# Kernel tuning notes

Hardware: AMD Instinct MI355X
Metric: run time of the kernel (lower is better)

The kernel has to match this reference:

```python
import jax, jax.numpy as jnp
import numpy as np

B, S, E = 2, 2048, 2048
H, HKV, KQV = 16, 4, 2048
D = KQV // H            # 128 head dim
KV_DIM = D * HKV        # 512
WINDOW = 256
NEG = jnp.finfo(jnp.float32).min


def setup_inputs() -> dict:
    key = jax.random.key(0)
    ks = jax.random.split(key, 5)
    sc = 0.02
    return {
        "hidden_states": jax.random.normal(ks[0], (B, S, E), jnp.float32),
        "Wq": jax.random.normal(ks[1], (KQV, E), jnp.float32) * sc,
        "Wk": jax.random.normal(ks[2], (KV_DIM, E), jnp.float32) * sc,
        "Wv": jax.random.normal(ks[3], (KV_DIM, E), jnp.float32) * sc,
        "Wo": jax.random.normal(ks[4], (E, KQV), jnp.float32) * sc,
        "bo": jnp.zeros((E,), jnp.float32),
    }


def reference(hidden_states, Wq, Wk, Wv, Wo, bo):
    x = hidden_states
    # projections (nn.Linear: x @ W.T)
    q = (x @ Wq.T).reshape(B, S, H, D).transpose(0, 2, 1, 3)      # [B,H,S,D]
    k = (x @ Wk.T).reshape(B, S, HKV, D).transpose(0, 2, 1, 3)    # [B,HKV,S,D]
    v = (x @ Wv.T).reshape(B, S, HKV, D).transpose(0, 2, 1, 3)

    # faithful reproduction of the module's index_select head expansion:
    # group_sizes are uniform (H % HKV == 0); both query and kv indices are
    # [0]*g + [1]*g + ... so query head i (i < HKV) is duplicated g times.
    idx = jnp.repeat(jnp.arange(HKV), H // HKV)                   # [H]
    qs = q[:, idx]                                                # [B,H,S,D]
    ks = k[:, idx]
    vs = v[:, idx]

    # GPT-Neo style: no 1/sqrt(D) scaling
    scores = jnp.einsum('bhqd,bhkd->bhqk', qs, ks)                # [B,H,S,S]

    i = jnp.arange(S)[:, None]
    j = jnp.arange(S)[None, :]
    # local causal mask: j <= i and j > i - WINDOW
    mask = (j <= i) & (j > i - WINDOW)                            # [S,S]
    scores = jnp.where(mask[None, None], scores, NEG)
    attn = jax.nn.softmax(scores, axis=-1)

    out = jnp.einsum('bhqk,bhkd->bhqd', attn, vs)                 # [B,H,S,D]
    out = out.transpose(0, 2, 1, 3).reshape(B, S, H * D)          # merge heads
    return out @ Wo.T + bo
```

## Files before the change

### kernel.cpp

```cpp
#include <hip/hip_runtime.h>

typedef _Float16 f16;
typedef _Float16 f16x8 __attribute__((ext_vector_type(8)));
typedef _Float16 f16x4 __attribute__((ext_vector_type(4)));
typedef float    f32x4 __attribute__((ext_vector_type(4)));


__device__ __forceinline__ void load_lds16(const void* g, void* l) {
    __builtin_amdgcn_global_load_lds(
        (__attribute__((address_space(1))) void*)(g),
        (__attribute__((address_space(3))) void*)(l), 16, 0, 0);
}

__global__ __launch_bounds__(256)
void cvt_pack(const float* __restrict__ X, const float* __restrict__ Wq,
              const float* __restrict__ Wk, const float* __restrict__ Wv,
              const float* __restrict__ Wo,
              f16* __restrict__ Xp, f16* __restrict__ Wp, f16* __restrict__ Wrp)
{
    const int blk = blockIdx.x, tid = threadIdx.x;
    if (blk < 4096) {
        int cid = blk * 256 + tid;
        int tile = cid >> 8, wc = cid & 255;
        int row = wc >> 2, kc = wc & 3;
        int m = ((tile >> 6) << 6) + row;
        int t = tile & 63;
        int sk = t * 32 + ((kc ^ ((row >> 1) & 3)) << 3);
        const float* s = X + (size_t)m * 2048 + sk;
        float4 a = *(const float4*)(s);
        float4 b = *(const float4*)(s + 4);
        f16x8 o;
        o[0]=(f16)a.x; o[1]=(f16)a.y; o[2]=(f16)a.z; o[3]=(f16)a.w;
        o[4]=(f16)b.x; o[5]=(f16)b.y; o[6]=(f16)b.z; o[7]=(f16)b.w;
        *(f16x8*)(Xp + (size_t)cid * 8) = o;
    } else if (blk < 5632) {
        int wid = (blk - 4096) * 256 + tid;
        int tile = wid >> 9, wc = wid & 511;
        int row = wc >> 2, kc = wc & 3;
        int n = ((tile >> 6) << 7) + row;
        int t = tile & 63;
        int sk = t * 32 + ((kc ^ ((row >> 1) & 3)) << 3);
        const float* src = (n < 512)  ? (Wq + (size_t)n * 2048 + sk)
                         : (n < 1024) ? (Wk + (size_t)(n - 512) * 2048 + sk)
                                      : (Wv + (size_t)(n - 1024) * 2048 + sk);
        float4 a = *(const float4*)(src);
        float4 b = *(const float4*)(src + 4);
        f16x8 o;
        o[0]=(f16)a.x; o[1]=(f16)a.y; o[2]=(f16)a.z; o[3]=(f16)a.w;
        o[4]=(f16)b.x; o[5]=(f16)b.y; o[6]=(f16)b.z; o[7]=(f16)b.w;
        *(f16x8*)(Wp + (size_t)wid * 8) = o;
    } else {
        int rid = (blk - 5632) * 256 + tid;
        int tile = rid >> 9, wc = rid & 511;
        int row = wc >> 2, kc = wc & 3;
        int e = ((tile >> 4) << 7) + row;
        int t = tile & 15;
        int cc = kc ^ ((row >> 1) & 3);
        int c = t * 32 + (cc << 3);
        int g = c >> 7, d0 = c & 127;
        const float* src = Wo + (size_t)e * 2048 + g * 512 + d0;
        float4 a0 = *(const float4*)(src);
        float4 a1 = *(const float4*)(src + 128);
        float4 a2 = *(const float4*)(src + 256);
        float4 a3 = *(const float4*)(src + 384);
        float4 b0 = *(const float4*)(src + 4);
        float4 b1 = *(const float4*)(src + 132);
        float4 b2 = *(const float4*)(src + 260);
        float4 b3 = *(const float4*)(src + 388);
        f16x8 o;
        o[0] = (f16)(a0.x + a1.x + a2.x + a3.x);
        o[1] = (f16)(a0.y + a1.y + a2.y + a3.y);
        o[2] = (f16)(a0.z + a1.z + a2.z + a3.z);
        o[3] = (f16)(a0.w + a1.w + a2.w + a3.w);
        o[4] = (f16)(b0.x + b1.x + b2.x + b3.x);
        o[5] = (f16)(b0.y + b1.y + b2.y + b3.y);
        o[6] = (f16)(b0.z + b1.z + b2.z + b3.z);
        o[7] = (f16)(b0.w + b1.w + b2.w + b3.w);
        *(f16x8*)(Wrp + (size_t)rid * 8) = o;
    }
}

__global__ __launch_bounds__(256)
void qkv_gemm(const f16* __restrict__ Xp, const f16* __restrict__ Wp,
              f16* __restrict__ Qo, f16* __restrict__ Ko, f16* __restrict__ Vo)
{
    const int NSTEP = 64;
    __shared__ __align__(16) f16 S[4][8192];

    const int tid = threadIdx.x;
    const int wave = tid >> 6, lane = tid & 63;
    const int lrow = lane & 15, lquad = lane >> 4;
    const int wr = wave >> 1, wc = wave & 1;

    int id = (int)blockIdx.x;
    int id2 = (id & 7) * 48 + (id >> 3);
    int bx = id2 % 12, by = id2 / 12;
    const int m0 = by * 128;

    const f16* gA0 = Xp + (size_t)(2 * by)     * 131072 + (size_t)tid * 8;
    const f16* gA1 = Xp + (size_t)(2 * by + 1) * 131072 + (size_t)tid * 8;
    const f16* gB0 = Wp + (size_t)bx * 262144 + (size_t)tid * 8;
    const f16* gB1 = Wp + (size_t)bx * 262144 + (size_t)(256 + tid) * 8;
    const int loA0 = tid * 8;
    const int loA1 = (256 + tid) * 8;
    const int loB0 = (512 + tid) * 8;
    const int loB1 = (768 + tid) * 8;

#define QSTAGE(t, buf)                                             \
    {                                                              \
        load_lds16(gA0 + (size_t)(t) * 2048, &S[buf][loA0]);       \
        load_lds16(gA1 + (size_t)(t) * 2048, &S[buf][loA1]);       \
        load_lds16(gB0 + (size_t)(t) * 4096, &S[buf][loB0]);       \
        load_lds16(gB1 + (size_t)(t) * 4096, &S[buf][loB1]);       \
    }

    int aoff[4], boff[4];
#pragma unroll
    for (int t = 0; t < 4; t++) {
        int ra = wr * 64 + t * 16 + lrow;
        aoff[t] = ra * 32 + ((lquad ^ ((ra >> 1) & 3)) << 3);
        int rb = wc * 64 + t * 16 + lrow;
        boff[t] = 4096 + rb * 32 + ((lquad ^ ((rb >> 1) & 3)) << 3);
    }

    f32x4 acc[4][4];
    const f32x4 z4 = {0.f, 0.f, 0.f, 0.f};
#pragma unroll
    for (int i = 0; i < 4; i++) for (int j = 0; j < 4; j++) acc[i][j] = z4;

    QSTAGE(0, 0); QSTAGE(1, 1); QSTAGE(2, 2);

    int buf = 0;
    for (int t = 0; t < NSTEP; ++t) {
        if (t < NSTEP - 2) {
            asm volatile("s_waitcnt vmcnt(8) lgkmcnt(0)" ::: "memory");
        } else if (t == NSTEP - 2) {
            asm volatile("s_waitcnt vmcnt(4) lgkmcnt(0)" ::: "memory");
        } else {
            asm volatile("s_waitcnt vmcnt(0) lgkmcnt(0)" ::: "memory");
        }
        __builtin_amdgcn_s_barrier();
        if (t < NSTEP - 3) QSTAGE(t + 3, (buf + 3) & 3);
        f16x8 af[4], bf[4];
#pragma unroll
        for (int mt = 0; mt < 4; mt++) af[mt] = *(const f16x8*)(&S[buf][aoff[mt]]);
#pragma unroll
        for (int nt = 0; nt < 4; nt++) bf[nt] = *(const f16x8*)(&S[buf][boff[nt]]);
#pragma unroll
        for (int mt = 0; mt < 4; mt++)
#pragma unroll
            for (int nt = 0; nt < 4; nt++)
                acc[mt][nt] = __builtin_amdgcn_mfma_f32_16x16x32_f16(af[mt], bf[nt], acc[mt][nt], 0, 0, 0);
        buf = (buf + 1) & 3;
    }
#undef QSTAGE

    const int z = bx >> 2;
    const int hh = bx & 3;
    if (z == 0) {
#pragma unroll
        for (int mt = 0; mt < 4; mt++) {
            int mbase = m0 + wr * 64 + mt * 16 + lquad * 4;
#pragma unroll
            for (int r = 0; r < 4; r++) {
                int m = mbase + r;
                int bb = m >> 11, s = m & 2047;
#pragma unroll
                for (int nt = 0; nt < 4; nt++) {
                    int d = wc * 64 + nt * 16 + lrow;
                    Qo[(size_t)(((bb * 4 + hh) << 11) + s) * 128 + d] = (f16)acc[mt][nt][r];
                }
            }
        }
    } else if (z == 1) {
#pragma unroll
        for (int mt = 0; mt < 4; mt++) {
            int mbase = m0 + wr * 64 + mt * 16 + lquad * 4;
#pragma unroll
            for (int r = 0; r < 4; r++) {
                int m = mbase + r;
                int bb = m >> 11, s = m & 2047;
                size_t base = ((size_t)(bb * 4 + hh) * 16 + (s >> 7)) * 16384
                            + (size_t)(s & 127) * 128;
#pragma unroll
                for (int nt = 0; nt < 4; nt++) {
                    int d = wc * 64 + nt * 16 + lrow;
                    Ko[base + (((d >> 3) ^ (s & 15)) << 3) + (d & 7)] = (f16)acc[mt][nt][r];
                }
            }
        }
    } else {
#pragma unroll
        for (int mt = 0; mt < 4; mt++) {
            int mbase = m0 + wr * 64 + mt * 16 + lquad * 4;
            int bb = mbase >> 11, s = mbase & 2047;
            int tt = s >> 7, sl = s & 127;
            int gsx = sl >> 3, j0 = sl & 7;
#pragma unroll
            for (int nt = 0; nt < 4; nt++) {
                int d = wc * 64 + nt * 16 + lrow;
                f16x4 pk;
#pragma unroll
                for (int r = 0; r < 4; r++) pk[r] = (f16)acc[mt][nt][r];
                *(f16x4*)(Vo + ((size_t)(bb * 4 + hh) * 16 + tt) * 16384
                             + (size_t)d * 128 + ((gsx ^ (d & 15)) << 3) + j0) = pk;
            }
        }
    }
}

__global__ __launch_bounds__(256)
void attn_win(const f16* __restrict__ Q, const f16* __restrict__ Kp,
              const f16* __restrict__ Vp, f16* __restrict__ AO)
{
    const int h = blockIdx.x;
    const int bg = h & 7, qt = h >> 3;
    const int b = bg >> 2, g = bg & 3;
    const int qbase = qt * 64;
    const int tid = threadIdx.x;
    const int wave = tid >> 6, lane = tid & 63;
    const int lrow = lane & 15, lquad = lane >> 4;
    const int qw = qbase + wave * 16;

    const f16* Qb = Q  + (size_t)bg * (2048 * 128);
    const f16* Kt = Kp + (size_t)bg * (2048 * 128);
    const f16* Vt = Vp + (size_t)bg * (2048 * 128);

    __shared__ __align__(16) f16 Ks[2][16384];
    __shared__ __align__(16) f16 Vs[2][16384];
    __shared__ __align__(16) f16 Pl[4][2048];

    f16x8 qf[4];
#pragma unroll
    for (int ks = 0; ks < 4; ks++)
        qf[ks] = *(const f16x8*)(Qb + (size_t)(qw + lrow) * 128 + ks * 32 + lquad * 8);

    float m_i[4], l_i[4];
    f32x4 oa[8];
    const f32x4 z4 = {0.f, 0.f, 0.f, 0.f};
#pragma unroll
    for (int r = 0; r < 4; r++) { m_i[r] = -30000.f; l_i[r] = 0.f; }
#pragma unroll
    for (int nt = 0; nt < 8; nt++) oa[nt] = z4;

    const int tstart = (qbase >= 256) ? ((qbase - 255) >> 7) : 0;
    const int tend = (qbase + 63) >> 7;

    {
        const f16* ksrc = Kt + (size_t)tstart * 16384;
        const f16* vsrc = Vt + (size_t)tstart * 16384;
#pragma unroll
        for (int j = 0; j < 8; j++) {
            load_lds16(ksrc + (j * 256 + tid) * 8, &Ks[0][(j * 256 + tid) * 8]);
            load_lds16(vsrc + (j * 256 + tid) * 8, &Vs[0][(j * 256 + tid) * 8]);
        }
    }

    int buf = 0;
    for (int t = tstart; t <= tend; ++t) {
        if (t < tend) {
            const f16* ksrc = Kt + (size_t)(t + 1) * 16384;
            const f16* vsrc = Vt + (size_t)(t + 1) * 16384;
#pragma unroll
            for (int j = 0; j < 8; j++) {
                load_lds16(ksrc + (j * 256 + tid) * 8, &Ks[buf ^ 1][(j * 256 + tid) * 8]);
                load_lds16(vsrc + (j * 256 + tid) * 8, &Vs[buf ^ 1][(j * 256 + tid) * 8]);
            }
            asm volatile("s_waitcnt vmcnt(16)" ::: "memory");
        } else {
            asm volatile("s_waitcnt vmcnt(0)" ::: "memory");
        }
        __builtin_amdgcn_s_barrier();

        const int kt = t * 128;
        f32x4 sc[8];
#pragma unroll
        for (int nt = 0; nt < 8; nt++) sc[nt] = z4;
#pragma unroll
        for (int nt = 0; nt < 8; nt++) {
#pragma unroll
            for (int ks = 0; ks < 4; ks++) {
                f16x8 kf = *(const f16x8*)(&Ks[buf][(nt * 16 + lrow) * 128
                                  + (((ks * 4 + lquad) ^ lrow) << 3)]);
                sc[nt] = __builtin_amdgcn_mfma_f32_16x16x32_f16(qf[ks], kf, sc[nt], 0, 0, 0);
            }
        }
#pragma unroll
        for (int r = 0; r < 4; r++) {
            const int qi = qw + lquad * 4 + r;
            float rmax = -60000.f;
#pragma unroll
            for (int nt = 0; nt < 8; nt++) {
                int kj = kt + nt * 16 + lrow;
                float sval = sc[nt][r];
                bool ok = (kj <= qi) && (kj + 256 > qi);
                sval = ok ? sval : -60000.f;
                sc[nt][r] = sval;
                rmax = fmaxf(rmax, sval);
            }
            rmax = fmaxf(rmax, __shfl_xor(rmax, 1));
            rmax = fmaxf(rmax, __shfl_xor(rmax, 2));
            rmax = fmaxf(rmax, __shfl_xor(rmax, 4));
            rmax = fmaxf(rmax, __shfl_xor(rmax, 8));
            float mold = m_i[r];
            float mnew = fmaxf(mold, rmax);
            float alpha = __expf(mold - mnew);
            m_i[r] = mnew;
            float rsum = 0.f;
#pragma unroll
            for (int nt = 0; nt < 8; nt++) {
                float p = __expf(sc[nt][r] - mnew);
                sc[nt][r] = p;
                rsum += p;
            }
            rsum += __shfl_xor(rsum, 1);
            rsum += __shfl_xor(rsum, 2);
            rsum += __shfl_xor(rsum, 4);
            rsum += __shfl_xor(rsum, 8);
            l_i[r] = l_i[r] * alpha + rsum;
#pragma unroll
            for (int nt = 0; nt < 8; nt++) oa[nt][r] *= alpha;
        }
#pragma unroll
        for (int nt = 0; nt < 8; nt++)
#pragma unroll
            for (int r = 0; r < 4; r++) {
                int row = lquad * 4 + r;
                int col = nt * 16 + lrow;
                Pl[wave][row * 128 + (((col >> 3) ^ row) << 3) + (col & 7)] = (f16)sc[nt][r];
            }
        f16x8 pf[4];
#pragma unroll
        for (int ks = 0; ks < 4; ks++)
            pf[ks] = *(const f16x8*)(&Pl[wave][lrow * 128
                              + (((ks * 4 + lquad) ^ lrow) << 3)]);
#pragma unroll
        for (int nt = 0; nt < 8; nt++) {
#pragma unroll
            for (int ks = 0; ks < 4; ks++) {
                f16x8 vf = *(const f16x8*)(&Vs[buf][(nt * 16 + lrow) * 128
                                  + (((ks * 4 + lquad) ^ lrow) << 3)]);
                oa[nt] = __builtin_amdgcn_mfma_f32_16x16x32_f16(pf[ks], vf, oa[nt], 0, 0, 0);
            }
        }
        asm volatile("s_waitcnt lgkmcnt(0)" ::: "memory");
        __builtin_amdgcn_s_barrier();
        buf ^= 1;
    }

    float inv[4];
#pragma unroll
    for (int r = 0; r < 4; r++) inv[r] = (l_i[r] > 0.f) ? 1.f / l_i[r] : 0.f;
#pragma unroll
    for (int nt = 0; nt < 8; nt++) {
#pragma unroll
        for (int r = 0; r < 4; r++) {
            int q = qw + lquad * 4 + r;
            int d = nt * 16 + lrow;
            int m = b * 2048 + q;
            int col = g * 128 + d;
            int p = m >> 6, r2 = m & 63;
            int tt = col >> 5;
            int cc = (col >> 3) & 3;
            size_t off = (((size_t)p * 16 + tt) * 64 + r2) * 32
                       + ((cc ^ ((r2 >> 1) & 3)) << 3) + (col & 7);
            AO[off] = (f16)(oa[nt][r] * inv[r]);
        }
    }
}

__global__ __launch_bounds__(256)
void out_gemm(const f16* __restrict__ Ap, const f16* __restrict__ Bp,
              const float* __restrict__ bias, float* __restrict__ C)
{
    const int NSTEP = 16, N = 2048;
    __shared__ __align__(16) f16 S[4][8192];

    const int tid = threadIdx.x;
    const int wave = tid >> 6, lane = tid & 63;
    const int lrow = lane & 15, lquad = lane >> 4;
    const int wr = wave >> 1, wc = wave & 1;

    int id = (int)blockIdx.x;
    int id2 = (id & 7) * 64 + (id >> 3);
    int bx = id2 & 15, by = id2 >> 4;
    const int m0 = by * 128, n0 = bx * 128;

    const f16* gA0 = Ap + (size_t)(2 * by)     * 32768 + (size_t)tid * 8;
    const f16* gA1 = Ap + (size_t)(2 * by + 1) * 32768 + (size_t)tid * 8;
    const f16* gB0 = Bp + (size_t)bx * 65536 + (size_t)tid * 8;
    const f16* gB1 = Bp + (size_t)bx * 65536 + (size_t)(256 + tid) * 8;
    const int loA0 = tid * 8;
    const int loA1 = (256 + tid) * 8;
    const int loB0 = (512 + tid) * 8;
    const int loB1 = (768 + tid) * 8;

#define OSTAGE(t, buf)                                             \
    {                                                              \
        load_lds16(gA0 + (size_t)(t) * 2048, &S[buf][loA0]);       \
        load_lds16(gA1 + (size_t)(t) * 2048, &S[buf][loA1]);       \
        load_lds16(gB0 + (size_t)(t) * 4096, &S[buf][loB0]);       \
        load_lds16(gB1 + (size_t)(t) * 4096, &S[buf][loB1]);       \
    }

    int aoff[4], boff[4];
#pragma unroll
    for (int t = 0; t < 4; t++) {
        int ra = wr * 64 + t * 16 + lrow;
        aoff[t] = ra * 32 + ((lquad ^ ((ra >> 1) & 3)) << 3);
        int rb = wc * 64 + t * 16 + lrow;
        boff[t] = 4096 + rb * 32 + ((lquad ^ ((rb >> 1) & 3)) << 3);
    }

    f32x4 acc[4][4];
    const f32x4 z4 = {0.f, 0.f, 0.f, 0.f};
#pragma unroll
    for (int i = 0; i < 4; i++) for (int j = 0; j < 4; j++) acc[i][j] = z4;

    OSTAGE(0, 0); OSTAGE(1, 1); OSTAGE(2, 2);

    int buf = 0;
    for (int t = 0; t < NSTEP; ++t) {
        if (t < NSTEP - 2) {
            asm volatile("s_waitcnt vmcnt(8) lgkmcnt(0)" ::: "memory");
        } else if (t == NSTEP - 2) {
            asm volatile("s_waitcnt vmcnt(4) lgkmcnt(0)" ::: "memory");
        } else {
            asm volatile("s_waitcnt vmcnt(0) lgkmcnt(0)" ::: "memory");
        }
        __builtin_amdgcn_s_barrier();
        if (t < NSTEP - 3) OSTAGE(t + 3, (buf + 3) & 3);
        f16x8 af[4], bf[4];
#pragma unroll
        for (int mt = 0; mt < 4; mt++) af[mt] = *(const f16x8*)(&S[buf][aoff[mt]]);
#pragma unroll
        for (int nt = 0; nt < 4; nt++) bf[nt] = *(const f16x8*)(&S[buf][boff[nt]]);
#pragma unroll
        for (int mt = 0; mt < 4; mt++)
#pragma unroll
            for (int nt = 0; nt < 4; nt++)
                acc[mt][nt] = __builtin_amdgcn_mfma_f32_16x16x32_f16(af[mt], bf[nt], acc[mt][nt], 0, 0, 0);
        buf = (buf + 1) & 3;
    }

#pragma unroll
    for (int nt = 0; nt < 4; nt++) {
        int n = n0 + wc * 64 + nt * 16 + lrow;
        float bv2 = bias[n];
#pragma unroll
        for (int mt = 0; mt < 4; mt++) {
            int mbase = m0 + wr * 64 + mt * 16 + lquad * 4;
#pragma unroll
            for (int r = 0; r < 4; r++)
                C[(size_t)(mbase + r) * N + n] = acc[mt][nt][r] + bv2;
        }
    }
#undef OSTAGE
}

extern "C" void kernel_launch(void* const* d_in, const int* in_sizes, int n_in,
                              void* d_out, int out_size, void* d_ws, size_t ws_size,
                              hipStream_t stream)
{
    const float* x  = (const float*)d_in[0];
    const float* Wq = (const float*)d_in[1];
    const float* Wk = (const float*)d_in[2];
    const float* Wv = (const float*)d_in[3];
    const float* Wo = (const float*)d_in[4];
    const float* bo = (const float*)d_in[5];
    float* out = (float*)d_out;

    f16* Xp  = (f16*)d_ws;
    f16* AO  = Xp;
    f16* Wp  = Xp  + 8388608;
    f16* Wrp = Wp  + 3145728;
    f16* Qws = Wrp + 1048576;
    f16* Kws = Qws + 2097152;
    f16* Vws = Kws + 2097152;

    cvt_pack<<<dim3(6144), 256, 0, stream>>>(x, Wq, Wk, Wv, Wo, Xp, Wp, Wrp);
    qkv_gemm<<<dim3(384), 256, 0, stream>>>(Xp, Wp, Qws, Kws, Vws);
    attn_win<<<dim3(256), 256, 0, stream>>>(Qws, Kws, Vws, AO);
    out_gemm<<<dim3(512), 256, 0, stream>>>(AO, Wrp, bo, out);
}
```

Measured before the change: 175.6 us.

## Split attention KV range across two wave halves with 64-key tiles and merge

The attention kernel now runs 512 threads per block. Each query group is handled by two waves that process alternating 64-key tiles, and their online-softmax states are merged at the end through LDS. V is stored in 64-key tiles with an adjusted swizzle, and K/V pairs are double-buffered with prefetch two steps ahead. The aim is more waves in flight and less masked work per 128-key tile, at the cost of an LDS merge step and an extra barrier.

```diff
diff --git a/kernel.cpp b/kernel.cpp
--- a/kernel.cpp
+++ b/kernel.cpp
@@ -194,7 +194,7 @@
         for (int mt = 0; mt < 4; mt++) {
             int mbase = m0 + wr * 64 + mt * 16 + lquad * 4;
             int bb = mbase >> 11, s = mbase & 2047;
-            int tt = s >> 7, sl = s & 127;
+            int tt = s >> 6, sl = s & 63;
             int gsx = sl >> 3, j0 = sl & 7;
 #pragma unroll
             for (int nt = 0; nt < 4; nt++) {
@@ -202,33 +202,34 @@
                 f16x4 pk;
 #pragma unroll
                 for (int r = 0; r < 4; r++) pk[r] = (f16)acc[mt][nt][r];
-                *(f16x4*)(Vo + ((size_t)(bb * 4 + hh) * 16 + tt) * 16384
-                             + (size_t)d * 128 + ((gsx ^ (d & 15)) << 3) + j0) = pk;
+                *(f16x4*)(Vo + ((size_t)(bb * 4 + hh) * 32 + tt) * 8192
+                             + (size_t)d * 64 + ((gsx ^ (d & 7)) << 3) + j0) = pk;
             }
         }
     }
 }
 
-__global__ __launch_bounds__(256)
+__global__ __launch_bounds__(512, 2)
 void attn_win(const f16* __restrict__ Q, const f16* __restrict__ Kp,
               const f16* __restrict__ Vp, f16* __restrict__ AO)
 {
-    const int h = blockIdx.x;
-    const int bg = h & 7, qt = h >> 3;
+    const int hblk = blockIdx.x;
+    const int bg = hblk & 7, qt = hblk >> 3;
     const int b = bg >> 2, g = bg & 3;
     const int qbase = qt * 64;
     const int tid = threadIdx.x;
     const int wave = tid >> 6, lane = tid & 63;
     const int lrow = lane & 15, lquad = lane >> 4;
-    const int qw = qbase + wave * 16;
+    const int qg = wave >> 1, hf = wave & 1;
+    const int qw = qbase + qg * 16;
 
     const f16* Qb = Q  + (size_t)bg * (2048 * 128);
-    const f16* Kt = Kp + (size_t)bg * (2048 * 128);
-    const f16* Vt = Vp + (size_t)bg * (2048 * 128);
-
-    __shared__ __align__(16) f16 Ks[2][16384];
-    __shared__ __align__(16) f16 Vs[2][16384];
-    __shared__ __align__(16) f16 Pl[4][2048];
+    const f16* Kt = Kp + (size_t)bg * 262144;
+    const f16* Vt = Vp + (size_t)bg * 262144;
+
+    __shared__ __align__(16) f16 Ks[2][2][8192];
+    __shared__ __align__(16) f16 Vs[2][2][8192];
+    __shared__ __align__(16) f16 Pl[8][1024];
 
     f16x8 qf[4];
 #pragma unroll
@@ -243,128 +244,165 @@
 #pragma unroll
     for (int nt = 0; nt < 8; nt++) oa[nt] = z4;
 
-    const int tstart = (qbase >= 256) ? ((qbase - 255) >> 7) : 0;
-    const int tend = (qbase + 63) >> 7;
-
-    {
-        const f16* ksrc = Kt + (size_t)tstart * 16384;
-        const f16* vsrc = Vt + (size_t)tstart * 16384;
-#pragma unroll
-        for (int j = 0; j < 8; j++) {
-            load_lds16(ksrc + (j * 256 + tid) * 8, &Ks[0][(j * 256 + tid) * 8]);
-            load_lds16(vsrc + (j * 256 + tid) * 8, &Vs[0][(j * 256 + tid) * 8]);
-        }
-    }
-
-    int buf = 0;
-    for (int t = tstart; t <= tend; ++t) {
-        if (t < tend) {
-            const f16* ksrc = Kt + (size_t)(t + 1) * 16384;
-            const f16* vsrc = Vt + (size_t)(t + 1) * 16384;
-#pragma unroll
-            for (int j = 0; j < 8; j++) {
-                load_lds16(ksrc + (j * 256 + tid) * 8, &Ks[buf ^ 1][(j * 256 + tid) * 8]);
-                load_lds16(vsrc + (j * 256 + tid) * 8, &Vs[buf ^ 1][(j * 256 + tid) * 8]);
-            }
-            asm volatile("s_waitcnt vmcnt(16)" ::: "memory");
-        } else {
-            asm volatile("s_waitcnt vmcnt(0)" ::: "memory");
-        }
+    const int t0v = (qbase >= 256) ? ((qbase - 255) >> 6) : 0;
+    const int t1v = (qbase + 63) >> 6;
+    const int T = t1v - t0v + 1;
+    const int I = (T + 1) >> 1;
+
+    const int c0 = (wave * 64 + lane) * 8;
+    const int c1 = c0 + 4096;
+
+#define APAIR(p, bufi)                                                         \
+    {                                                                          \
+        int tA = t0v + 2 * (p);  if (tA > t1v) tA = t1v;                       \
+        int tB = tA + 1;         if (tB > t1v) tB = t1v;                       \
+        const f16* kA = Kt + (size_t)(tA >> 1) * 16384 + (size_t)(tA & 1) * 8192; \
+        const f16* vA = Vt + (size_t)tA * 8192;                                \
+        const f16* kB = Kt + (size_t)(tB >> 1) * 16384 + (size_t)(tB & 1) * 8192; \
+        const f16* vB = Vt + (size_t)tB * 8192;                                \
+        load_lds16(kA + c0, &Ks[0][bufi][c0]);                                 \
+        load_lds16(kA + c1, &Ks[0][bufi][c1]);                                 \
+        load_lds16(vA + c0, &Vs[0][bufi][c0]);                                 \
+        load_lds16(vA + c1, &Vs[0][bufi][c1]);                                 \
+        load_lds16(kB + c0, &Ks[1][bufi][c0]);                                 \
+        load_lds16(kB + c1, &Ks[1][bufi][c1]);                                 \
+        load_lds16(vB + c0, &Vs[1][bufi][c0]);                                 \
+        load_lds16(vB + c1, &Vs[1][bufi][c1]);                                 \
+    }
+
+    APAIR(0, 0);
+    APAIR(1, 1);
+
+    int bufc = 0;
+    for (int i = 0; i < I; ++i) {
+        if (i < I - 1) asm volatile("s_waitcnt vmcnt(8)" ::: "memory");
+        else           asm volatile("s_waitcnt vmcnt(0)" ::: "memory");
         __builtin_amdgcn_s_barrier();
 
-        const int kt = t * 128;
-        f32x4 sc[8];
-#pragma unroll
-        for (int nt = 0; nt < 8; nt++) sc[nt] = z4;
-#pragma unroll
-        for (int nt = 0; nt < 8; nt++) {
-#pragma unroll
-            for (int ks = 0; ks < 4; ks++) {
-                f16x8 kf = *(const f16x8*)(&Ks[buf][(nt * 16 + lrow) * 128
-                                  + (((ks * 4 + lquad) ^ lrow) << 3)]);
-                sc[nt] = __builtin_amdgcn_mfma_f32_16x16x32_f16(qf[ks], kf, sc[nt], 0, 0, 0);
-            }
-        }
-#pragma unroll
-        for (int r = 0; r < 4; r++) {
-            const int qi = qw + lquad * 4 + r;
-            float rmax = -60000.f;
+        const int t = t0v + 2 * i + hf;
+        if (t <= t1v) {
+            const int kt = t * 64;
+            f32x4 sc[4];
+#pragma unroll
+            for (int nt = 0; nt < 4; nt++) sc[nt] = z4;
+#pragma unroll
+            for (int nt = 0; nt < 4; nt++) {
+#pragma unroll
+                for (int ks = 0; ks < 4; ks++) {
+                    f16x8 kf = *(const f16x8*)(&Ks[hf][bufc][(nt * 16 + lrow) * 128
+                                      + (((ks * 4 + lquad) ^ lrow) << 3)]);
+                    sc[nt] = __builtin_amdgcn_mfma_f32_16x16x32_f16(qf[ks], kf, sc[nt], 0, 0, 0);
+                }
+            }
+#pragma unroll
+            for (int r = 0; r < 4; r++) {
+                const int qi = qw + lquad * 4 + r;
+                float rmax = -60000.f;
+#pragma unroll
+                for (int nt = 0; nt < 4; nt++) {
+                    int kj = kt + nt * 16 + lrow;
+                    float sval = sc[nt][r];
+                    bool ok = (kj <= qi) && (kj + 256 > qi);
+                    sval = ok ? sval : -60000.f;
+                    sc[nt][r] = sval;
+                    rmax = fmaxf(rmax, sval);
+                }
+                rmax = fmaxf(rmax, __shfl_xor(rmax, 1));
+                rmax = fmaxf(rmax, __shfl_xor(rmax, 2));
+                rmax = fmaxf(rmax, __shfl_xor(rmax, 4));
+                rmax = fmaxf(rmax, __shfl_xor(rmax, 8));
+                float mold = m_i[r];
+                float mnew = fmaxf(mold, rmax);
+                float alpha = __expf(mold - mnew);
+                m_i[r] = mnew;
+                float rsum = 0.f;
+#pragma unroll
+                for (int nt = 0; nt < 4; nt++) {
+                    float p = __expf(sc[nt][r] - mnew);
+                    sc[nt][r] = p;
+                    rsum += p;
+                }
+                rsum += __shfl_xor(rsum, 1);
+                rsum += __shfl_xor(rsum, 2);
+                rsum += __shfl_xor(rsum, 4);
+                rsum += __shfl_xor(rsum, 8);
+                l_i[r] = l_i[r] * alpha + rsum;
+#pragma unroll
+                for (int nt = 0; nt < 8; nt++) oa[nt][r] *= alpha;
+            }
+#pragma unroll
+            for (int nt = 0; nt < 4; nt++)
+#pragma unroll
+                for (int r = 0; r < 4; r++) {
+                    int row = lquad * 4 + r;
+                    Pl[wave][row * 64 + (((nt * 2 + (lrow >> 3)) ^ (row & 7)) << 3)
+                             + (lrow & 7)] = (f16)sc[nt][r];
+                }
+            f16x8 pf[2];
+#pragma unroll
+            for (int ks = 0; ks < 2; ks++)
+                pf[ks] = *(const f16x8*)(&Pl[wave][lrow * 64
+                                  + (((ks * 4 + lquad) ^ (lrow & 7)) << 3)]);
 #pragma unroll
             for (int nt = 0; nt < 8; nt++) {
-                int kj = kt + nt * 16 + lrow;
-                float sval = sc[nt][r];
-                bool ok = (kj <= qi) && (kj + 256 > qi);
-                sval = ok ? sval : -60000.f;
-                sc[nt][r] = sval;
-                rmax = fmaxf(rmax, sval);
-            }
-            rmax = fmaxf(rmax, __shfl_xor(rmax, 1));
-            rmax = fmaxf(rmax, __shfl_xor(rmax, 2));
-            rmax = fmaxf(rmax, __shfl_xor(rmax, 4));
-            rmax = fmaxf(rmax, __shfl_xor(rmax, 8));
-            float mold = m_i[r];
-            float mnew = fmaxf(mold, rmax);
-            float alpha = __expf(mold - mnew);
-            m_i[r] = mnew;
-            float rsum = 0.f;
-#pragma unroll
-            for (int nt = 0; nt < 8; nt++) {
-                float p = __expf(sc[nt][r] - mnew);
-                sc[nt][r] = p;
-                rsum += p;
-            }
-            rsum += __shfl_xor(rsum, 1);
-            rsum += __shfl_xor(rsum, 2);
-            rsum += __shfl_xor(rsum, 4);
-            rsum += __shfl_xor(rsum, 8);
-            l_i[r] = l_i[r] * alpha + rsum;
-#pragma unroll
-            for (int nt = 0; nt < 8; nt++) oa[nt][r] *= alpha;
-        }
-#pragma unroll
-        for (int nt = 0; nt < 8; nt++)
-#pragma unroll
-            for (int r = 0; r < 4; r++) {
-                int row = lquad * 4 + r;
-                int col = nt * 16 + lrow;
-                Pl[wave][row * 128 + (((col >> 3) ^ row) << 3) + (col & 7)] = (f16)sc[nt][r];
-            }
-        f16x8 pf[4];
-#pragma unroll
-        for (int ks = 0; ks < 4; ks++)
-            pf[ks] = *(const f16x8*)(&Pl[wave][lrow * 128
-                              + (((ks * 4 + lquad) ^ lrow) << 3)]);
-#pragma unroll
-        for (int nt = 0; nt < 8; nt++) {
-#pragma unroll
-            for (int ks = 0; ks < 4; ks++) {
-                f16x8 vf = *(const f16x8*)(&Vs[buf][(nt * 16 + lrow) * 128
-                                  + (((ks * 4 + lquad) ^ lrow) << 3)]);
-                oa[nt] = __builtin_amdgcn_mfma_f32_16x16x32_f16(pf[ks], vf, oa[nt], 0, 0, 0);
+#pragma unroll
+                for (int ks = 0; ks < 2; ks++) {
+                    int dv = nt * 16 + lrow;
+                    f16x8 vf = *(const f16x8*)(&Vs[hf][bufc][dv * 64
+                                      + (((ks * 4 + lquad) ^ (dv & 7)) << 3)]);
+                    oa[nt] = __builtin_amdgcn_mfma_f32_16x16x32_f16(pf[ks], vf, oa[nt], 0, 0, 0);
+                }
             }
         }
         asm volatile("s_waitcnt lgkmcnt(0)" ::: "memory");
         __builtin_amdgcn_s_barrier();
-        buf ^= 1;
-    }
-
-    float inv[4];
-#pragma unroll
-    for (int r = 0; r < 4; r++) inv[r] = (l_i[r] > 0.f) ? 1.f / l_i[r] : 0.f;
-#pragma unroll
-    for (int nt = 0; nt < 8; nt++) {
+        if (i + 2 < I) APAIR(i + 2, bufc);
+        bufc ^= 1;
+    }
+#undef APAIR
+
+    float* mrg = (float*)&Ks[0][0][0];
+    if (hf == 1) {
 #pragma unroll
         for (int r = 0; r < 4; r++) {
-            int q = qw + lquad * 4 + r;
-            int d = nt * 16 + lrow;
+            int row = lquad * 4 + r;
+            if (lrow == 0) {
+                mrg[qg * 16 + row] = m_i[r];
+                mrg[64 + qg * 16 + row] = l_i[r];
+            }
+#pragma unroll
+            for (int nt = 0; nt < 8; nt++)
+                mrg[128 + qg * 2048 + row * 128 + nt * 16 + lrow] = oa[nt][r];
+        }
+    }
+    asm volatile("s_waitcnt lgkmcnt(0)" ::: "memory");
+    __builtin_amdgcn_s_barrier();
+    if (hf == 0) {
+#pragma unroll
+        for (int r = 0; r < 4; r++) {
+            int row = lquad * 4 + r;
+            float m1 = mrg[qg * 16 + row];
+            float l1 = mrg[64 + qg * 16 + row];
+            float mm = fmaxf(m_i[r], m1);
+            float a0 = __expf(m_i[r] - mm);
+            float a1 = __expf(m1 - mm);
+            float ll = l_i[r] * a0 + l1 * a1;
+            float inv = (ll > 0.f) ? 1.f / ll : 0.f;
+            int q = qw + row;
             int m = b * 2048 + q;
-            int col = g * 128 + d;
             int p = m >> 6, r2 = m & 63;
-            int tt = col >> 5;
-            int cc = (col >> 3) & 3;
-            size_t off = (((size_t)p * 16 + tt) * 64 + r2) * 32
-                       + ((cc ^ ((r2 >> 1) & 3)) << 3) + (col & 7);
-            AO[off] = (f16)(oa[nt][r] * inv[r]);
+#pragma unroll
+            for (int nt = 0; nt < 8; nt++) {
+                int d = nt * 16 + lrow;
+                float o1 = mrg[128 + qg * 2048 + row * 128 + d];
+                float od = (oa[nt][r] * a0 + o1 * a1) * inv;
+                int col = g * 128 + d;
+                int tt = col >> 5;
+                int cc = (col >> 3) & 3;
+                size_t off = (((size_t)p * 16 + tt) * 64 + r2) * 32
+                           + ((cc ^ ((r2 >> 1) & 3)) << 3) + (col & 7);
+                AO[off] = (f16)od;
+            }
         }
     }
 }
@@ -480,6 +518,6 @@
 
     cvt_pack<<<dim3(6144), 256, 0, stream>>>(x, Wq, Wk, Wv, Wo, Xp, Wp, Wrp);
     qkv_gemm<<<dim3(384), 256, 0, stream>>>(Xp, Wp, Qws, Kws, Vws);
-    attn_win<<<dim3(256), 256, 0, stream>>>(Qws, Kws, Vws, AO);
+    attn_win<<<dim3(256), 512, 0, stream>>>(Qws, Kws, Vws, AO);
     out_gemm<<<dim3(512), 256, 0, stream>>>(AO, Wrp, bo, out);
 }
```

After: 175.1 us. No clear change (-0.3%).
